# Kernel optimization log

Hardware: AMD Instinct MI355X
Metric: run time of the kernel (lower is better)

Reference implementation:

```python
import jax, jax.numpy as jnp
import numpy as np
from jax import lax

NX, NW, NY, NLAYER = 128, 64, 32, 2
NWUP, NBATCH, NHRZN = 256, 1024, 256


def setup_inputs() -> dict:
    key = jax.random.key(0)
    ks = jax.random.split(key, 18)
    s = 0.05
    n = lambda k, shp: jax.random.normal(k, shp, jnp.float32) * s
    return {
        "_Y0": jax.random.normal(ks[0], (NWUP + 1, NBATCH, NY), jnp.float32),
        # q_x_y: Linear(Ny, Nx*Nlayer) + Tanh
        "Wq": n(ks[1], (NX * NLAYER, NY)), "bq": n(ks[2], (NX * NLAYER,)),
        # p_y_x: Linear(Nx,Nx)+Tanh+Linear(Nx,Ny)
        "Wp1": n(ks[3], (NX, NX)), "bp1": n(ks[4], (NX,)),
        "Wp2": n(ks[5], (NY, NX)), "bp2": n(ks[6], (NY,)),
        # q_w_xy: Linear(Nx+Ny, Nw)+Tanh
        "Ww": n(ks[7], (NW, NX + NY)), "bw": n(ks[8], (NW,)),
        # GRU layer 0 (input Nw) and layer 1 (input Nx), PyTorch gate order r,z,n
        "Wih0": n(ks[9], (3 * NX, NW)), "Whh0": n(ks[10], (3 * NX, NX)),
        "bih0": n(ks[11], (3 * NX,)), "bhh0": n(ks[12], (3 * NX,)),
        "Wih1": n(ks[13], (3 * NX, NX)), "Whh1": n(ks[14], (3 * NX, NX)),
        "bih1": n(ks[15], (3 * NX,)), "bhh1": n(ks[16], (3 * NX,)),
        "Nhrzn": NHRZN,
    }


def _gru_cell(x, h, Wih, Whh, bih, bhh):
    # PyTorch GRUCell math, gate order (r, z, n)
    gi = x @ Wih.T + bih
    gh = h @ Whh.T + bhh
    ir, iz, inn = jnp.split(gi, 3, axis=-1)
    hr, hz, hn = jnp.split(gh, 3, axis=-1)
    r = jax.nn.sigmoid(ir + hr)
    z = jax.nn.sigmoid(iz + hz)
    ng = jnp.tanh(inn + r * hn)
    return (1.0 - z) * ng + z * h


def reference(_Y0, Wq, bq, Wp1, bp1, Wp2, bp2, Ww, bw,
              Wih0, Whh0, bih0, bhh0, Wih1, Whh1, bih1, bhh1, Nhrzn):
    Nwup = _Y0.shape[0] - 1
    B, Ny = _Y0.shape[1], _Y0.shape[2]
    Nlayer = Wq.shape[0] // Wp1.shape[0]
    Nx = Wp1.shape[0]

    p_y_x = lambda h: jnp.tanh(h @ Wp1.T + bp1) @ Wp2.T + bp2

    # initial multi-layer hidden state (Nlayer, B, Nx)
    x0 = jnp.tanh(_Y0[0] @ Wq.T + bq).reshape(B, Nlayer, Nx).transpose(1, 0, 2)
    yhat0 = p_y_x(x0[-1])

    T = Nwup + Nhrzn
    y_seq = jnp.concatenate(
        [_Y0[1:], jnp.zeros((Nhrzn, B, Ny), _Y0.dtype)], axis=0)  # (T, B, Ny)
    wup_mask = (jnp.arange(T) < Nwup).astype(_Y0.dtype)  # training branch: w=0 in horizon

    def step(carry, inp):
        x, yhat = carry  # x: (Nlayer, B, Nx)
        y_t, m = inp
        e = y_t - yhat
        w = jnp.tanh(jnp.concatenate([x[0], e], axis=-1) @ Ww.T + bw) * m
        h0 = _gru_cell(w, x[0], Wih0, Whh0, bih0, bhh0)
        h1 = _gru_cell(h0, x[1], Wih1, Whh1, bih1, bhh1)
        x_new = jnp.stack([h0, h1], axis=0)
        yhat_new = p_y_x(h1)
        return (x_new, yhat_new), (h1, w, yhat_new)

    _, (Xs, Ws, Ys) = lax.scan(step, (x0, yhat0), (y_seq, wup_mask))

    X = jnp.concatenate([x0[-1][None], Xs], axis=0)      # (T+1, B, Nx)
    Yhat = jnp.concatenate([yhat0[None], Ys], axis=0)    # (T+1, B, Ny)
    W = Ws[:Nwup]                                        # (Nwup, B, Nw)
    return X, W, Yhat
```

## Files before the change

kernel.cpp:

```cpp
#include <hip/hip_runtime.h>

#define NBATCH 1024
#define TSTEPS 512
#define NWUPC  256

#define XLEN 67239936ULL
#define WLEN 16777216ULL

typedef __attribute__((ext_vector_type(8))) short bf16x8;
typedef __attribute__((ext_vector_type(4))) float f32x4;

__device__ __forceinline__ unsigned short to_bf16u(float f) {
  union { float f; unsigned u; } v; v.f = f;
  unsigned r = (v.u + 0x7FFFu + ((v.u >> 16) & 1u)) >> 16;
  return (unsigned short)r;
}
__device__ __forceinline__ float bf16_to_f(short h) {
  union { unsigned u; float f; } v;
  v.u = ((unsigned)(unsigned short)h) << 16;
  return v.f;
}
__device__ __forceinline__ float sigm(float x) {
  x = fminf(fmaxf(x, -30.f), 30.f);
  return __builtin_amdgcn_rcpf(1.f + __expf(-x));
}
__device__ __forceinline__ float ftanh(float x) {
  x = fminf(fmaxf(x, -15.f), 15.f);
  float e = __expf(2.f * x);
  return (e - 1.f) * __builtin_amdgcn_rcpf(e + 1.f);
}

#define MFMA16(a, b, c) __builtin_amdgcn_mfma_f32_16x16x32_bf16((a), (b), (c), 0, 0, 0)

__device__ __forceinline__ bf16x8 load_wfrag(const float* __restrict__ W, int ldk,
                                             int rowbase, int kbase, int cl, int rg) {
  const float* p = W + (size_t)(rowbase + cl) * (size_t)ldk + (size_t)(kbase + rg * 8);
  float4 a = *reinterpret_cast<const float4*>(p);
  float4 b = *reinterpret_cast<const float4*>(p + 4);
  bf16x8 r;
  r[0] = (short)to_bf16u(a.x); r[1] = (short)to_bf16u(a.y);
  r[2] = (short)to_bf16u(a.z); r[3] = (short)to_bf16u(a.w);
  r[4] = (short)to_bf16u(b.x); r[5] = (short)to_bf16u(b.y);
  r[6] = (short)to_bf16u(b.z); r[7] = (short)to_bf16u(b.w);
  return r;
}

template <int ROWB, int SLOTS>
__device__ __forceinline__ bf16x8 lds_afrag(const unsigned short* buf, int kt, int cl, int rg) {
  int chunk = (kt * 4 + rg) ^ (cl & (SLOTS - 1));
  return *reinterpret_cast<const bf16x8*>(
      reinterpret_cast<const char*>(buf) + cl * ROWB + chunk * 16);
}

template <int ROWB, int SLOTS>
__device__ __forceinline__ void store_c_lds(unsigned short* buf, int colbase, f32x4 v,
                                            int cl, int rg) {
#pragma unroll
  for (int r = 0; r < 4; ++r) {
    int row = rg * 4 + r;
    int col = colbase + cl;
    int chunk = (col >> 3) ^ (row & (SLOTS - 1));
    *reinterpret_cast<unsigned short*>(
        reinterpret_cast<char*>(buf) + row * ROWB + chunk * 16 + (col & 7) * 2) =
        to_bf16u(v[r]);
  }
}

__device__ __forceinline__ void store_c_glb(float* __restrict__ base, int ld, int colbase,
                                            f32x4 v, int cl, int rg) {
#pragma unroll
  for (int r = 0; r < 4; ++r) base[(rg * 4 + r) * ld + colbase + cl] = v[r];
}

__device__ __forceinline__ bf16x8 read_pfrag(const unsigned short* buf, int f, int lane) {
  return *reinterpret_cast<const bf16x8*>(buf + f * 512 + lane * 8);
}

__global__ __launch_bounds__(256, 1) void sinkbf_kernel(
    const float* __restrict__ Y0, const float* __restrict__ Wq, const float* __restrict__ bq,
    const float* __restrict__ Wp1, const float* __restrict__ bp1,
    const float* __restrict__ Wp2, const float* __restrict__ bp2,
    const float* __restrict__ Ww, const float* __restrict__ bw,
    const float* __restrict__ Wih0, const float* __restrict__ Whh0,
    const float* __restrict__ bih0, const float* __restrict__ bhh0,
    const float* __restrict__ Wih1, const float* __restrict__ Whh1,
    const float* __restrict__ bih1, const float* __restrict__ bhh1,
    float* __restrict__ outX, float* __restrict__ outW, float* __restrict__ outY) {
  const int tid = threadIdx.x;
  const int wid = tid >> 6;
  const int lane = tid & 63;
  const int cl = lane & 15;
  const int rg = lane >> 4;
  const int row0 = blockIdx.x * 16;
  const int c0 = wid * 32;

  __shared__ __align__(16) unsigned short sH0[2][16 * 128];
  __shared__ __align__(16) unsigned short sH1[2][16 * 128];
  __shared__ __align__(16) unsigned short sWb[16 * 64];
  __shared__ __align__(16) unsigned short sT[16 * 128];
  __shared__ __align__(16) unsigned short sYh[16 * 32];
  __shared__ __align__(16) unsigned short sWwP[20 * 512];
  __shared__ __align__(16) unsigned short sWp1P[32 * 512];
  __shared__ __align__(16) unsigned short sWp2P[8 * 512];

  const f32x4 vzero = {0.f, 0.f, 0.f, 0.f};

  bf16x8 wI0[3][2][2];
  bf16x8 wH0[3][2][4];
  bf16x8 wI1[3][2][4];
  bf16x8 wH1[3][2][4];
#pragma unroll
  for (int g = 0; g < 3; ++g) {
#pragma unroll
    for (int tl = 0; tl < 2; ++tl) {
      int rb = g * 128 + c0 + tl * 16;
#pragma unroll
      for (int kt = 0; kt < 2; ++kt) wI0[g][tl][kt] = load_wfrag(Wih0, 64, rb, kt * 32, cl, rg);
#pragma unroll
      for (int kt = 0; kt < 4; ++kt) wH0[g][tl][kt] = load_wfrag(Whh0, 128, rb, kt * 32, cl, rg);
#pragma unroll
      for (int kt = 0; kt < 4; ++kt) wI1[g][tl][kt] = load_wfrag(Wih1, 128, rb, kt * 32, cl, rg);
#pragma unroll
      for (int kt = 0; kt < 4; ++kt) wH1[g][tl][kt] = load_wfrag(Whh1, 128, rb, kt * 32, cl, rg);
    }
  }

#pragma unroll
  for (int kt = 0; kt < 5; ++kt) {
    bf16x8 f = load_wfrag(Ww, 160, wid * 16, kt * 32, cl, rg);
    *reinterpret_cast<bf16x8*>(&sWwP[(wid * 5 + kt) * 512 + lane * 8]) = f;
  }
#pragma unroll
  for (int tl = 0; tl < 2; ++tl)
#pragma unroll
    for (int kt = 0; kt < 4; ++kt) {
      bf16x8 f = load_wfrag(Wp1, 128, c0 + tl * 16, kt * 32, cl, rg);
      *reinterpret_cast<bf16x8*>(&sWp1P[((wid * 2 + tl) * 4 + kt) * 512 + lane * 8]) = f;
    }
  if (wid < 2) {
#pragma unroll
    for (int kt = 0; kt < 4; ++kt) {
      bf16x8 f = load_wfrag(Wp2, 128, wid * 16, kt * 32, cl, rg);
      *reinterpret_cast<bf16x8*>(&sWp2P[(wid * 4 + kt) * 512 + lane * 8]) = f;
    }
  }

  float b0r[2], b0z[2], b0in[2], b0hn[2], b1r[2], b1z[2], b1in[2], b1hn[2], bp1l[2];
#pragma unroll
  for (int tl = 0; tl < 2; ++tl) {
    int c = c0 + tl * 16 + cl;
    b0r[tl] = bih0[c] + bhh0[c];
    b0z[tl] = bih0[128 + c] + bhh0[128 + c];
    b0in[tl] = bih0[256 + c];
    b0hn[tl] = bhh0[256 + c];
    b1r[tl] = bih1[c] + bhh1[c];
    b1z[tl] = bih1[128 + c] + bhh1[128 + c];
    b1in[tl] = bih1[256 + c];
    b1hn[tl] = bhh1[256 + c];
    bp1l[tl] = bp1[c];
  }
  const float bwl = bw[wid * 16 + cl];
  const float bp2l = (wid < 2) ? bp2[wid * 16 + cl] : 0.f;

  f32x4 hp0[2], hp1[2];

  {
    bf16x8 aY = load_wfrag(Y0, 32, row0, 0, cl, rg);
#pragma unroll
    for (int tl = 0; tl < 2; ++tl) {
      bf16x8 q0 = load_wfrag(Wq, 32, c0 + tl * 16, 0, cl, rg);
      bf16x8 q1 = load_wfrag(Wq, 32, 128 + c0 + tl * 16, 0, cl, rg);
      float bq0v = bq[c0 + tl * 16 + cl];
      float bq1v = bq[128 + c0 + tl * 16 + cl];
      f32x4 acc = MFMA16(aY, q0, vzero);
#pragma unroll
      for (int r = 0; r < 4; ++r) hp0[tl][r] = ftanh(acc[r] + bq0v);
      store_c_lds<256, 8>(sH0[0], c0 + tl * 16, hp0[tl], cl, rg);
      acc = MFMA16(aY, q1, vzero);
#pragma unroll
      for (int r = 0; r < 4; ++r) hp1[tl][r] = ftanh(acc[r] + bq1v);
      store_c_lds<256, 8>(sH1[0], c0 + tl * 16, hp1[tl], cl, rg);
      store_c_glb(outX + (size_t)row0 * 128, 128, c0 + tl * 16, hp1[tl], cl, rg);
    }
  }
  __syncthreads();

  auto p_phase = [&](int tout, const unsigned short* h1buf) {
    bf16x8 a1[4];
#pragma unroll
    for (int kt = 0; kt < 4; ++kt) a1[kt] = lds_afrag<256, 8>(h1buf, kt, cl, rg);
#pragma unroll
    for (int tl = 0; tl < 2; ++tl) {
      f32x4 acc = vzero;
#pragma unroll
      for (int kt = 0; kt < 4; ++kt)
        acc = MFMA16(a1[kt], read_pfrag(sWp1P, (wid * 2 + tl) * 4 + kt, lane), acc);
      f32x4 tv;
#pragma unroll
      for (int r = 0; r < 4; ++r) tv[r] = ftanh(acc[r] + bp1l[tl]);
      store_c_lds<256, 8>(sT, c0 + tl * 16, tv, cl, rg);
    }
    __syncthreads();
    if (wid < 2) {
      bf16x8 at[4];
#pragma unroll
      for (int kt = 0; kt < 4; ++kt) at[kt] = lds_afrag<256, 8>(sT, kt, cl, rg);
      f32x4 acc = vzero;
#pragma unroll
      for (int kt = 0; kt < 4; ++kt) acc = MFMA16(at[kt], read_pfrag(sWp2P, wid * 4 + kt, lane), acc);
      f32x4 y;
#pragma unroll
      for (int r = 0; r < 4; ++r) y[r] = acc[r] + bp2l;
      store_c_glb(outY + (size_t)tout * (NBATCH * 32) + (size_t)row0 * 32, 32, wid * 16, y, cl, rg);
      store_c_lds<64, 4>(sYh, wid * 16, y, cl, rg);
    }
    __syncthreads();
  };

  p_phase(0, sH1[0]);

#pragma unroll 1
  for (int t = 0; t < TSTEPS; ++t) {
    const int cur = t & 1, nxt = cur ^ 1;
    const unsigned short* h0c = sH0[cur];
    unsigned short* h0w = sH0[nxt];
    const unsigned short* h1c = sH1[cur];
    unsigned short* h1w = sH1[nxt];

    bf16x8 aH0[4];
#pragma unroll
    for (int kt = 0; kt < 4; ++kt) aH0[kt] = lds_afrag<256, 8>(h0c, kt, cl, rg);

    if (t < NWUPC) {
      bf16x8 ae;
      {
        const float* py = Y0 + (size_t)(1 + t) * (NBATCH * 32) + (size_t)(row0 + cl) * 32 + rg * 8;
        float4 ya = *reinterpret_cast<const float4*>(py);
        float4 yb = *reinterpret_cast<const float4*>(py + 4);
        int chunk = rg ^ (cl & 3);
        bf16x8 yh = *reinterpret_cast<const bf16x8*>(
            reinterpret_cast<const char*>(sYh) + cl * 64 + chunk * 16);
        ae[0] = (short)to_bf16u(ya.x - bf16_to_f(yh[0]));
        ae[1] = (short)to_bf16u(ya.y - bf16_to_f(yh[1]));
        ae[2] = (short)to_bf16u(ya.z - bf16_to_f(yh[2]));
        ae[3] = (short)to_bf16u(ya.w - bf16_to_f(yh[3]));
        ae[4] = (short)to_bf16u(yb.x - bf16_to_f(yh[4]));
        ae[5] = (short)to_bf16u(yb.y - bf16_to_f(yh[5]));
        ae[6] = (short)to_bf16u(yb.z - bf16_to_f(yh[6]));
        ae[7] = (short)to_bf16u(yb.w - bf16_to_f(yh[7]));
      }
      f32x4 acc = vzero;
#pragma unroll
      for (int kt = 0; kt < 4; ++kt) acc = MFMA16(aH0[kt], read_pfrag(sWwP, wid * 5 + kt, lane), acc);
      acc = MFMA16(ae, read_pfrag(sWwP, wid * 5 + 4, lane), acc);
      f32x4 wv;
#pragma unroll
      for (int r = 0; r < 4; ++r) wv[r] = ftanh(acc[r] + bwl);
      store_c_lds<128, 8>(sWb, wid * 16, wv, cl, rg);
      store_c_glb(outW + (size_t)t * (NBATCH * 64) + (size_t)row0 * 64, 64, wid * 16, wv, cl, rg);
      __syncthreads();
    }

    f32x4 ar[2], az[2], ain[2], ahn[2];
#pragma unroll
    for (int tl = 0; tl < 2; ++tl) { ar[tl] = vzero; az[tl] = vzero; ain[tl] = vzero; ahn[tl] = vzero; }
    if (t < NWUPC) {
      bf16x8 aw0 = lds_afrag<128, 8>(sWb, 0, cl, rg);
      bf16x8 aw1 = lds_afrag<128, 8>(sWb, 1, cl, rg);
#pragma unroll
      for (int tl = 0; tl < 2; ++tl) {
        ar[tl] = MFMA16(aw0, wI0[0][tl][0], ar[tl]);  ar[tl] = MFMA16(aw1, wI0[0][tl][1], ar[tl]);
        az[tl] = MFMA16(aw0, wI0[1][tl][0], az[tl]);  az[tl] = MFMA16(aw1, wI0[1][tl][1], az[tl]);
        ain[tl] = MFMA16(aw0, wI0[2][tl][0], ain[tl]); ain[tl] = MFMA16(aw1, wI0[2][tl][1], ain[tl]);
      }
    }
#pragma unroll
    for (int kt = 0; kt < 4; ++kt)
#pragma unroll
      for (int tl = 0; tl < 2; ++tl) {
        ar[tl] = MFMA16(aH0[kt], wH0[0][tl][kt], ar[tl]);
        az[tl] = MFMA16(aH0[kt], wH0[1][tl][kt], az[tl]);
        ahn[tl] = MFMA16(aH0[kt], wH0[2][tl][kt], ahn[tl]);
      }
    f32x4 h0new[2];
#pragma unroll
    for (int tl = 0; tl < 2; ++tl)
#pragma unroll
      for (int r = 0; r < 4; ++r) {
        float rr = sigm(ar[tl][r] + b0r[tl]);
        float zz = sigm(az[tl][r] + b0z[tl]);
        float ng = ftanh(ain[tl][r] + b0in[tl] + rr * (ahn[tl][r] + b0hn[tl]));
        h0new[tl][r] = (1.f - zz) * ng + zz * hp0[tl][r];
      }
#pragma unroll
    for (int tl = 0; tl < 2; ++tl) {
      store_c_lds<256, 8>(h0w, c0 + tl * 16, h0new[tl], cl, rg);
      hp0[tl] = h0new[tl];
    }
    __syncthreads();

    bf16x8 aH0n[4], aH1[4];
#pragma unroll
    for (int kt = 0; kt < 4; ++kt) aH0n[kt] = lds_afrag<256, 8>(h0w, kt, cl, rg);
#pragma unroll
    for (int kt = 0; kt < 4; ++kt) aH1[kt] = lds_afrag<256, 8>(h1c, kt, cl, rg);
#pragma unroll
    for (int tl = 0; tl < 2; ++tl) { ar[tl] = vzero; az[tl] = vzero; ain[tl] = vzero; ahn[tl] = vzero; }
#pragma unroll
    for (int kt = 0; kt < 4; ++kt)
#pragma unroll
      for (int tl = 0; tl < 2; ++tl) {
        ar[tl] = MFMA16(aH0n[kt], wI1[0][tl][kt], ar[tl]);
        az[tl] = MFMA16(aH0n[kt], wI1[1][tl][kt], az[tl]);
        ain[tl] = MFMA16(aH0n[kt], wI1[2][tl][kt], ain[tl]);
        ar[tl] = MFMA16(aH1[kt], wH1[0][tl][kt], ar[tl]);
        az[tl] = MFMA16(aH1[kt], wH1[1][tl][kt], az[tl]);
        ahn[tl] = MFMA16(aH1[kt], wH1[2][tl][kt], ahn[tl]);
      }
    f32x4 h1new[2];
#pragma unroll
    for (int tl = 0; tl < 2; ++tl)
#pragma unroll
      for (int r = 0; r < 4; ++r) {
        float rr = sigm(ar[tl][r] + b1r[tl]);
        float zz = sigm(az[tl][r] + b1z[tl]);
        float ng = ftanh(ain[tl][r] + b1in[tl] + rr * (ahn[tl][r] + b1hn[tl]));
        h1new[tl][r] = (1.f - zz) * ng + zz * hp1[tl][r];
      }
#pragma unroll
    for (int tl = 0; tl < 2; ++tl) {
      store_c_lds<256, 8>(h1w, c0 + tl * 16, h1new[tl], cl, rg);
      store_c_glb(outX + (size_t)(1 + t) * (NBATCH * 128) + (size_t)row0 * 128, 128,
                  c0 + tl * 16, h1new[tl], cl, rg);
      hp1[tl] = h1new[tl];
    }
    __syncthreads();

    p_phase(1 + t, h1w);
  }
}

extern "C" void kernel_launch(void* const* d_in, const int* in_sizes, int n_in,
                              void* d_out, int out_size, void* d_ws, size_t ws_size,
                              hipStream_t stream) {
  (void)in_sizes; (void)n_in; (void)out_size; (void)d_ws; (void)ws_size;
  const float* Y0   = (const float*)d_in[0];
  const float* Wq   = (const float*)d_in[1];
  const float* bq   = (const float*)d_in[2];
  const float* Wp1  = (const float*)d_in[3];
  const float* bp1  = (const float*)d_in[4];
  const float* Wp2  = (const float*)d_in[5];
  const float* bp2  = (const float*)d_in[6];
  const float* Ww   = (const float*)d_in[7];
  const float* bw   = (const float*)d_in[8];
  const float* Wih0 = (const float*)d_in[9];
  const float* Whh0 = (const float*)d_in[10];
  const float* bih0 = (const float*)d_in[11];
  const float* bhh0 = (const float*)d_in[12];
  const float* Wih1 = (const float*)d_in[13];
  const float* Whh1 = (const float*)d_in[14];
  const float* bih1 = (const float*)d_in[15];
  const float* bhh1 = (const float*)d_in[16];

  float* outX = (float*)d_out;
  float* outW = outX + XLEN;
  float* outY = outW + WLEN;

  sinkbf_kernel<<<dim3(NBATCH / 16), dim3(256), 0, stream>>>(
      Y0, Wq, bq, Wp1, bp1, Wp2, bp2, Ww, bw,
      Wih0, Whh0, bih0, bhh0, Wih1, Whh1, bih1, bhh1,
      outX, outW, outY);
}
```

Baseline: 2.022 ms.

## Move horizon yhat projection to a parallel kernel and overlap GRU matmuls

During the horizon steps the predicted output does not feed the recurrence, because the masked innovation term is zero. The recurrent kernel therefore skips the p_y_x projection and its two barriers for those steps. A second, fully parallel kernel recomputes Yhat for the horizon from the stored X. The layer-1 hidden-state matmuls are also issued early, next to the layer-0 and W matmuls, and the next step's Y0 is prefetched into registers. __syncthreads is replaced by a barrier that only waits on LDS counters. The cost is a second launch that re-reads X from global memory, plus more live accumulator registers.

Result: slower. 2.363 ms (+16.9%).

```diff
diff --git a/kernel.cpp b/kernel.cpp
--- a/kernel.cpp
+++ b/kernel.cpp
@@ -28,6 +28,13 @@
   x = fminf(fmaxf(x, -15.f), 15.f);
   float e = __expf(2.f * x);
   return (e - 1.f) * __builtin_amdgcn_rcpf(e + 1.f);
+}
+
+__device__ __forceinline__ void fast_barrier() {
+  __builtin_amdgcn_sched_barrier(0);
+  asm volatile("s_waitcnt lgkmcnt(0)" ::: "memory");
+  __builtin_amdgcn_s_barrier();
+  __builtin_amdgcn_sched_barrier(0);
 }
 
 #define MFMA16(a, b, c) __builtin_amdgcn_mfma_f32_16x16x32_bf16((a), (b), (c), 0, 0, 0)
@@ -185,6 +192,13 @@
   }
   __syncthreads();
 
+  float4 yA, yB;
+  {
+    const float* py = Y0 + (size_t)1 * (NBATCH * 32) + (size_t)(row0 + cl) * 32 + rg * 8;
+    yA = *reinterpret_cast<const float4*>(py);
+    yB = *reinterpret_cast<const float4*>(py + 4);
+  }
+
   auto p_phase = [&](int tout, const unsigned short* h1buf) {
     bf16x8 a1[4];
 #pragma unroll
@@ -200,7 +214,7 @@
       for (int r = 0; r < 4; ++r) tv[r] = ftanh(acc[r] + bp1l[tl]);
       store_c_lds<256, 8>(sT, c0 + tl * 16, tv, cl, rg);
     }
-    __syncthreads();
+    fast_barrier();
     if (wid < 2) {
       bf16x8 at[4];
 #pragma unroll
@@ -214,7 +228,7 @@
       store_c_glb(outY + (size_t)tout * (NBATCH * 32) + (size_t)row0 * 32, 32, wid * 16, y, cl, rg);
       store_c_lds<64, 4>(sYh, wid * 16, y, cl, rg);
     }
-    __syncthreads();
+    fast_barrier();
   };
 
   p_phase(0, sH1[0]);
@@ -226,70 +240,93 @@
     unsigned short* h0w = sH0[nxt];
     const unsigned short* h1c = sH1[cur];
     unsigned short* h1w = sH1[nxt];
-
-    bf16x8 aH0[4];
+    const bool warm = (t < NWUPC);
+
+    bf16x8 aH0[4], aH1[4];
 #pragma unroll
     for (int kt = 0; kt < 4; ++kt) aH0[kt] = lds_afrag<256, 8>(h0c, kt, cl, rg);
-
-    if (t < NWUPC) {
+#pragma unroll
+    for (int kt = 0; kt < 4; ++kt) aH1[kt] = lds_afrag<256, 8>(h1c, kt, cl, rg);
+
+    f32x4 ar0[2], az0[2], ain0[2], ahn0[2];
+    f32x4 ar1[2], az1[2], ahn1[2];
+#pragma unroll
+    for (int tl = 0; tl < 2; ++tl) {
+      ar0[tl] = vzero; az0[tl] = vzero; ain0[tl] = vzero; ahn0[tl] = vzero;
+      ar1[tl] = vzero; az1[tl] = vzero; ahn1[tl] = vzero;
+    }
+
+    if (warm) {
       bf16x8 ae;
       {
-        const float* py = Y0 + (size_t)(1 + t) * (NBATCH * 32) + (size_t)(row0 + cl) * 32 + rg * 8;
-        float4 ya = *reinterpret_cast<const float4*>(py);
-        float4 yb = *reinterpret_cast<const float4*>(py + 4);
         int chunk = rg ^ (cl & 3);
         bf16x8 yh = *reinterpret_cast<const bf16x8*>(
             reinterpret_cast<const char*>(sYh) + cl * 64 + chunk * 16);
-        ae[0] = (short)to_bf16u(ya.x - bf16_to_f(yh[0]));
-        ae[1] = (short)to_bf16u(ya.y - bf16_to_f(yh[1]));
-        ae[2] = (short)to_bf16u(ya.z - bf16_to_f(yh[2]));
-        ae[3] = (short)to_bf16u(ya.w - bf16_to_f(yh[3]));
-        ae[4] = (short)to_bf16u(yb.x - bf16_to_f(yh[4]));
-        ae[5] = (short)to_bf16u(yb.y - bf16_to_f(yh[5]));
-        ae[6] = (short)to_bf16u(yb.z - bf16_to_f(yh[6]));
-        ae[7] = (short)to_bf16u(yb.w - bf16_to_f(yh[7]));
+        ae[0] = (short)to_bf16u(yA.x - bf16_to_f(yh[0]));
+        ae[1] = (short)to_bf16u(yA.y - bf16_to_f(yh[1]));
+        ae[2] = (short)to_bf16u(yA.z - bf16_to_f(yh[2]));
+        ae[3] = (short)to_bf16u(yA.w - bf16_to_f(yh[3]));
+        ae[4] = (short)to_bf16u(yB.x - bf16_to_f(yh[4]));
+        ae[5] = (short)to_bf16u(yB.y - bf16_to_f(yh[5]));
+        ae[6] = (short)to_bf16u(yB.z - bf16_to_f(yh[6]));
+        ae[7] = (short)to_bf16u(yB.w - bf16_to_f(yh[7]));
+      }
+      if (t + 1 < NWUPC) {
+        const float* py = Y0 + (size_t)(2 + t) * (NBATCH * 32) + (size_t)(row0 + cl) * 32 + rg * 8;
+        yA = *reinterpret_cast<const float4*>(py);
+        yB = *reinterpret_cast<const float4*>(py + 4);
       }
       f32x4 acc = vzero;
 #pragma unroll
       for (int kt = 0; kt < 4; ++kt) acc = MFMA16(aH0[kt], read_pfrag(sWwP, wid * 5 + kt, lane), acc);
       acc = MFMA16(ae, read_pfrag(sWwP, wid * 5 + 4, lane), acc);
+#pragma unroll
+      for (int kt = 0; kt < 4; ++kt)
+#pragma unroll
+        for (int tl = 0; tl < 2; ++tl) {
+          ar0[tl] = MFMA16(aH0[kt], wH0[0][tl][kt], ar0[tl]);
+          az0[tl] = MFMA16(aH0[kt], wH0[1][tl][kt], az0[tl]);
+          ahn0[tl] = MFMA16(aH0[kt], wH0[2][tl][kt], ahn0[tl]);
+          ar1[tl] = MFMA16(aH1[kt], wH1[0][tl][kt], ar1[tl]);
+          az1[tl] = MFMA16(aH1[kt], wH1[1][tl][kt], az1[tl]);
+          ahn1[tl] = MFMA16(aH1[kt], wH1[2][tl][kt], ahn1[tl]);
+        }
       f32x4 wv;
 #pragma unroll
       for (int r = 0; r < 4; ++r) wv[r] = ftanh(acc[r] + bwl);
       store_c_lds<128, 8>(sWb, wid * 16, wv, cl, rg);
       store_c_glb(outW + (size_t)t * (NBATCH * 64) + (size_t)row0 * 64, 64, wid * 16, wv, cl, rg);
-      __syncthreads();
-    }
-
-    f32x4 ar[2], az[2], ain[2], ahn[2];
-#pragma unroll
-    for (int tl = 0; tl < 2; ++tl) { ar[tl] = vzero; az[tl] = vzero; ain[tl] = vzero; ahn[tl] = vzero; }
-    if (t < NWUPC) {
+      fast_barrier();
       bf16x8 aw0 = lds_afrag<128, 8>(sWb, 0, cl, rg);
       bf16x8 aw1 = lds_afrag<128, 8>(sWb, 1, cl, rg);
 #pragma unroll
       for (int tl = 0; tl < 2; ++tl) {
-        ar[tl] = MFMA16(aw0, wI0[0][tl][0], ar[tl]);  ar[tl] = MFMA16(aw1, wI0[0][tl][1], ar[tl]);
-        az[tl] = MFMA16(aw0, wI0[1][tl][0], az[tl]);  az[tl] = MFMA16(aw1, wI0[1][tl][1], az[tl]);
-        ain[tl] = MFMA16(aw0, wI0[2][tl][0], ain[tl]); ain[tl] = MFMA16(aw1, wI0[2][tl][1], ain[tl]);
-      }
-    }
-#pragma unroll
-    for (int kt = 0; kt < 4; ++kt)
-#pragma unroll
-      for (int tl = 0; tl < 2; ++tl) {
-        ar[tl] = MFMA16(aH0[kt], wH0[0][tl][kt], ar[tl]);
-        az[tl] = MFMA16(aH0[kt], wH0[1][tl][kt], az[tl]);
-        ahn[tl] = MFMA16(aH0[kt], wH0[2][tl][kt], ahn[tl]);
-      }
+        ar0[tl] = MFMA16(aw0, wI0[0][tl][0], ar0[tl]);  ar0[tl] = MFMA16(aw1, wI0[0][tl][1], ar0[tl]);
+        az0[tl] = MFMA16(aw0, wI0[1][tl][0], az0[tl]);  az0[tl] = MFMA16(aw1, wI0[1][tl][1], az0[tl]);
+        ain0[tl] = MFMA16(aw0, wI0[2][tl][0], ain0[tl]); ain0[tl] = MFMA16(aw1, wI0[2][tl][1], ain0[tl]);
+      }
+    } else {
+#pragma unroll
+      for (int kt = 0; kt < 4; ++kt)
+#pragma unroll
+        for (int tl = 0; tl < 2; ++tl) {
+          ar0[tl] = MFMA16(aH0[kt], wH0[0][tl][kt], ar0[tl]);
+          az0[tl] = MFMA16(aH0[kt], wH0[1][tl][kt], az0[tl]);
+          ahn0[tl] = MFMA16(aH0[kt], wH0[2][tl][kt], ahn0[tl]);
+          ar1[tl] = MFMA16(aH1[kt], wH1[0][tl][kt], ar1[tl]);
+          az1[tl] = MFMA16(aH1[kt], wH1[1][tl][kt], az1[tl]);
+          ahn1[tl] = MFMA16(aH1[kt], wH1[2][tl][kt], ahn1[tl]);
+        }
+    }
+
     f32x4 h0new[2];
 #pragma unroll
     for (int tl = 0; tl < 2; ++tl)
 #pragma unroll
       for (int r = 0; r < 4; ++r) {
-        float rr = sigm(ar[tl][r] + b0r[tl]);
-        float zz = sigm(az[tl][r] + b0z[tl]);
-        float ng = ftanh(ain[tl][r] + b0in[tl] + rr * (ahn[tl][r] + b0hn[tl]));
+        float rr = sigm(ar0[tl][r] + b0r[tl]);
+        float zz = sigm(az0[tl][r] + b0z[tl]);
+        float ng = ftanh(ain0[tl][r] + b0in[tl] + rr * (ahn0[tl][r] + b0hn[tl]));
         h0new[tl][r] = (1.f - zz) * ng + zz * hp0[tl][r];
       }
 #pragma unroll
@@ -297,34 +334,30 @@
       store_c_lds<256, 8>(h0w, c0 + tl * 16, h0new[tl], cl, rg);
       hp0[tl] = h0new[tl];
     }
-    __syncthreads();
-
-    bf16x8 aH0n[4], aH1[4];
+    fast_barrier();
+
+    bf16x8 aH0n[4];
 #pragma unroll
     for (int kt = 0; kt < 4; ++kt) aH0n[kt] = lds_afrag<256, 8>(h0w, kt, cl, rg);
-#pragma unroll
-    for (int kt = 0; kt < 4; ++kt) aH1[kt] = lds_afrag<256, 8>(h1c, kt, cl, rg);
-#pragma unroll
-    for (int tl = 0; tl < 2; ++tl) { ar[tl] = vzero; az[tl] = vzero; ain[tl] = vzero; ahn[tl] = vzero; }
+    f32x4 ain1[2];
+#pragma unroll
+    for (int tl = 0; tl < 2; ++tl) ain1[tl] = vzero;
 #pragma unroll
     for (int kt = 0; kt < 4; ++kt)
 #pragma unroll
       for (int tl = 0; tl < 2; ++tl) {
-        ar[tl] = MFMA16(aH0n[kt], wI1[0][tl][kt], ar[tl]);
-        az[tl] = MFMA16(aH0n[kt], wI1[1][tl][kt], az[tl]);
-        ain[tl] = MFMA16(aH0n[kt], wI1[2][tl][kt], ain[tl]);
-        ar[tl] = MFMA16(aH1[kt], wH1[0][tl][kt], ar[tl]);
-        az[tl] = MFMA16(aH1[kt], wH1[1][tl][kt], az[tl]);
-        ahn[tl] = MFMA16(aH1[kt], wH1[2][tl][kt], ahn[tl]);
+        ar1[tl] = MFMA16(aH0n[kt], wI1[0][tl][kt], ar1[tl]);
+        az1[tl] = MFMA16(aH0n[kt], wI1[1][tl][kt], az1[tl]);
+        ain1[tl] = MFMA16(aH0n[kt], wI1[2][tl][kt], ain1[tl]);
       }
     f32x4 h1new[2];
 #pragma unroll
     for (int tl = 0; tl < 2; ++tl)
 #pragma unroll
       for (int r = 0; r < 4; ++r) {
-        float rr = sigm(ar[tl][r] + b1r[tl]);
-        float zz = sigm(az[tl][r] + b1z[tl]);
-        float ng = ftanh(ain[tl][r] + b1in[tl] + rr * (ahn[tl][r] + b1hn[tl]));
+        float rr = sigm(ar1[tl][r] + b1r[tl]);
+        float zz = sigm(az1[tl][r] + b1z[tl]);
+        float ng = ftanh(ain1[tl][r] + b1in[tl] + rr * (ahn1[tl][r] + b1hn[tl]));
         h1new[tl][r] = (1.f - zz) * ng + zz * hp1[tl][r];
       }
 #pragma unroll
@@ -334,9 +367,74 @@
                   c0 + tl * 16, h1new[tl], cl, rg);
       hp1[tl] = h1new[tl];
     }
+    fast_barrier();
+
+    if (warm) p_phase(1 + t, h1w);
+  }
+}
+
+__global__ __launch_bounds__(256, 1) void yhat_hrzn_kernel(
+    const float* __restrict__ X, const float* __restrict__ Wp1, const float* __restrict__ bp1,
+    const float* __restrict__ Wp2, const float* __restrict__ bp2, float* __restrict__ outY) {
+  const int tid = threadIdx.x;
+  const int wid = tid >> 6;
+  const int lane = tid & 63;
+  const int cl = lane & 15;
+  const int rg = lane >> 4;
+  const int tile = blockIdx.x & 63;
+  const int tg = blockIdx.x >> 6;
+  const int row0 = tile * 16;
+  const int c0 = wid * 32;
+
+  __shared__ __align__(16) unsigned short sT2[2][16 * 128];
+  const f32x4 vzero = {0.f, 0.f, 0.f, 0.f};
+
+  bf16x8 wp1f[2][4];
+#pragma unroll
+  for (int tl = 0; tl < 2; ++tl)
+#pragma unroll
+    for (int kt = 0; kt < 4; ++kt) wp1f[tl][kt] = load_wfrag(Wp1, 128, c0 + tl * 16, kt * 32, cl, rg);
+  bf16x8 wp2f[4];
+  if (wid < 2) {
+#pragma unroll
+    for (int kt = 0; kt < 4; ++kt) wp2f[kt] = load_wfrag(Wp2, 128, wid * 16, kt * 32, cl, rg);
+  } else {
+#pragma unroll
+    for (int kt = 0; kt < 4; ++kt) wp2f[kt] = bf16x8{0, 0, 0, 0, 0, 0, 0, 0};
+  }
+  float bp1l[2] = {bp1[c0 + cl], bp1[c0 + 16 + cl]};
+  const float bp2l = (wid < 2) ? bp2[wid * 16 + cl] : 0.f;
+
+#pragma unroll 1
+  for (int i = 0; i < 4; ++i) {
+    const int tt = 257 + tg * 4 + i;
+    const float* xb = X + (size_t)tt * (NBATCH * 128);
+    bf16x8 aX[4];
+#pragma unroll
+    for (int kt = 0; kt < 4; ++kt) aX[kt] = load_wfrag(xb, 128, row0, kt * 32, cl, rg);
+#pragma unroll
+    for (int tl = 0; tl < 2; ++tl) {
+      f32x4 acc = vzero;
+#pragma unroll
+      for (int kt = 0; kt < 4; ++kt) acc = MFMA16(aX[kt], wp1f[tl][kt], acc);
+      f32x4 tv;
+#pragma unroll
+      for (int r = 0; r < 4; ++r) tv[r] = ftanh(acc[r] + bp1l[tl]);
+      store_c_lds<256, 8>(sT2[i & 1], c0 + tl * 16, tv, cl, rg);
+    }
     __syncthreads();
-
-    p_phase(1 + t, h1w);
+    if (wid < 2) {
+      bf16x8 at[4];
+#pragma unroll
+      for (int kt = 0; kt < 4; ++kt) at[kt] = lds_afrag<256, 8>(sT2[i & 1], kt, cl, rg);
+      f32x4 acc = vzero;
+#pragma unroll
+      for (int kt = 0; kt < 4; ++kt) acc = MFMA16(at[kt], wp2f[kt], acc);
+      f32x4 y;
+#pragma unroll
+      for (int r = 0; r < 4; ++r) y[r] = acc[r] + bp2l;
+      store_c_glb(outY + (size_t)tt * (NBATCH * 32) + (size_t)row0 * 32, 32, wid * 16, y, cl, rg);
+    }
   }
 }
 
@@ -370,4 +468,7 @@
       Y0, Wq, bq, Wp1, bp1, Wp2, bp2, Ww, bw,
       Wih0, Whh0, bih0, bhh0, Wih1, Whh1, bih1, bhh1,
       outX, outW, outY);
-}
+
+  yhat_hrzn_kernel<<<dim3(64 * 64), dim3(256), 0, stream>>>(
+      outX, Wp1, bp1, Wp2, bp2, outY);
+}
```
